# Optimization experiments

Hardware: AMD Instinct MI355X
Metric: run time of the kernel (lower is better)

The kernel has to match this reference:

```python
import jax, jax.numpy as jnp
import numpy as np

B, L, D, H, DK, DV, FF, V, N = 1, 1024, 1024, 16, 64, 64, 4096, 32000, 12


def _ln(x, s, b):
    mu = jnp.mean(x, axis=-1, keepdims=True)
    var = jnp.mean((x - mu) ** 2, axis=-1, keepdims=True)
    return (x - mu) / jnp.sqrt(var + 1e-5) * s + b


def _pe(length, d):
    # interleaved sin/cos positional encoding, matching stack([sin,cos],-1).view(L,D)
    i = 2.0 * jnp.arange(d // 2, dtype=jnp.float32)
    base = 10000.0 ** (-i / d)
    half = jnp.arange(length, dtype=jnp.float32)[:, None] * base[None, :]  # [L, D/2]
    return jnp.stack([jnp.sin(half), jnp.cos(half)], axis=-1).reshape(length, d)


def setup_inputs() -> dict:
    key = jax.random.key(0)
    ks = jax.random.split(key, 8)
    s = 0.02
    return {
        "tokens": jax.random.randint(ks[0], (B, L), 0, V),
        "emb": jax.random.normal(ks[1], (V, D), jnp.float32) * s,
        "final_b": jnp.zeros((V,), jnp.float32),
        "Wq": jax.random.normal(ks[2], (N, H, D, DK), jnp.float32) * s,
        "Wk": jax.random.normal(ks[3], (N, H, D, DK), jnp.float32) * s,
        "Wv": jax.random.normal(ks[4], (N, H, D, DV), jnp.float32) * s,
        "Wo": jax.random.normal(ks[5], (N, H * DV, D), jnp.float32) * s,
        "ln1_s": jnp.ones((N, D), jnp.float32),
        "ln1_b": jnp.zeros((N, D), jnp.float32),
        "W1": jax.random.normal(ks[6], (N, D, FF), jnp.float32) * s,
        "b1": jnp.zeros((N, FF), jnp.float32),
        "W2": jax.random.normal(ks[7], (N, FF, D), jnp.float32) * s,
        "b2": jnp.zeros((N, D), jnp.float32),
        "ln2_s": jnp.ones((N, D), jnp.float32),
        "ln2_b": jnp.zeros((N, D), jnp.float32),
    }


def _forward(tokens, emb, final_b, Wq, Wk, Wv, Wo, ln1_s, ln1_b, W1, b1, W2, b2, ln2_s, ln2_b):
    a = emb[tokens] * jnp.sqrt(jnp.float32(3.0 * D))  # tied-weight scaling
    a = a + (a + _pe(L, D))  # faithful to `a += pe(a)` where pe returns x + PE
    mask = jnp.tril(jnp.ones((L, L), dtype=bool))
    scale = 1.0 / jnp.sqrt(jnp.float32(D))  # original divides by sqrt(d_model), not d_k

    def layer(x, p):
        wq, wk, wv, wo, s1, sb1, w1, bb1, w2, bb2, s2, sb2 = p
        q = jnp.einsum('bld,hdk->bhlk', x, wq)
        k = jnp.einsum('bld,hdk->bhlk', x, wk)
        v = jnp.einsum('bld,hdv->bhlv', x, wv)
        scores = jnp.einsum('bhqk,bhmk->bhqm', q, k) * scale  # [B,H,L,L]
        scores = jnp.where(mask, scores, -jnp.inf)  # causal triu(-inf)
        attn = jax.nn.softmax(scores, axis=-1)
        o = jnp.einsum('bhqm,bhmv->bhqv', attn, v)
        o = o.transpose(0, 2, 1, 3).reshape(x.shape[0], L, H * DV)  # concat heads
        x = _ln(x + o @ wo, s1, sb1)  # post-LN residual
        f = jax.nn.relu(x @ w1 + bb1) @ w2 + bb2
        x = _ln(x + f, s2, sb2)
        return x, None

    x, _ = jax.lax.scan(layer, a, (Wq, Wk, Wv, Wo, ln1_s, ln1_b, W1, b1, W2, b2, ln2_s, ln2_b))
    return x @ emb.T + final_b  # tied output projection with bias


def reference(tokens, emb, final_b, Wq, Wk, Wv, Wo, ln1_s, ln1_b, W1, b1, W2, b2, ln2_s, ln2_b):
    return _forward(tokens, emb, final_b, Wq, Wk, Wv, Wo, ln1_s, ln1_b, W1, b1, W2, b2, ln2_s, ln2_b)
```

## Files before the change

kernel.cpp:

```cpp
#include <hip/hip_runtime.h>

typedef unsigned short u16;
typedef __attribute__((ext_vector_type(8))) short short8;
typedef __attribute__((ext_vector_type(4))) float f32x4;
typedef __attribute__((ext_vector_type(4))) u16 u16x4;

#define LSEQ   1024
#define DMODEL 1024
#define NHEAD  16
#define DHEAD  64
#define DFF    4096
#define NLAYER 12
#define NVOCAB 32000

__device__ __forceinline__ u16 f2b(float f) {
  union { float f; unsigned u; } x; x.f = f;
  unsigned r = x.u + 0x7fffu + ((x.u >> 16) & 1u);
  return (u16)(r >> 16);
}
__device__ __forceinline__ float b2f(u16 u) {
  union { unsigned u; float f; } x; x.u = ((unsigned)u) << 16; return x.f;
}

__device__ __forceinline__ f32x4 mfma16(short8 a, short8 b, f32x4 c) {
  return __builtin_amdgcn_mfma_f32_16x16x32_bf16(a, b, c, 0, 0, 0);
}

__device__ __forceinline__ void gload16(const u16* g, u16* l) {
  __builtin_amdgcn_global_load_lds(
      (const __attribute__((address_space(1))) void*)g,
      (__attribute__((address_space(3))) void*)l, 16, 0, 0);
}

template<int N> __device__ __forceinline__ void waitvm() {
  if constexpr (N <= 0)      asm volatile("s_waitcnt vmcnt(0)" ::: "memory");
  else if constexpr (N == 1) asm volatile("s_waitcnt vmcnt(1)" ::: "memory");
  else if constexpr (N == 2) asm volatile("s_waitcnt vmcnt(2)" ::: "memory");
  else if constexpr (N == 3) asm volatile("s_waitcnt vmcnt(3)" ::: "memory");
  else if constexpr (N == 4) asm volatile("s_waitcnt vmcnt(4)" ::: "memory");
  else if constexpr (N == 5) asm volatile("s_waitcnt vmcnt(5)" ::: "memory");
  else if constexpr (N == 6) asm volatile("s_waitcnt vmcnt(6)" ::: "memory");
  else                       asm volatile("s_waitcnt vmcnt(8)" ::: "memory");
}

__global__ __launch_bounds__(256) void embed_k(const int* __restrict__ tok,
    const float* __restrict__ emb, float* __restrict__ x, u16* __restrict__ xb)
{
  const int l = blockIdx.x;
  const int d0 = threadIdx.x * 4;
  const int t = tok[l];
  const float lf = (float)l;
  float o[4]; u16 obv[4];
#pragma unroll
  for (int j = 0; j < 4; ++j) {
    int d = d0 + j;
    int p = d >> 1;
    float ang = lf * powf(10000.0f, -(float)(2 * p) / 1024.0f);
    float pe = (d & 1) ? cosf(ang) : sinf(ang);
    float val = 2.0f * emb[(size_t)t * DMODEL + d] * 55.42562584220407f + pe;
    o[j] = val; obv[j] = f2b(val);
  }
  *reinterpret_cast<float4*>(x + (size_t)l * DMODEL + d0) = make_float4(o[0], o[1], o[2], o[3]);
  u16x4 vb = { obv[0], obv[1], obv[2], obv[3] };
  *reinterpret_cast<u16x4*>(xb + (size_t)l * DMODEL + d0) = vb;
}

__global__ __launch_bounds__(256) void ln_k(const float* __restrict__ xin,
    const float* __restrict__ ypart, int P, const float* __restrict__ ybias,
    const float* __restrict__ s, const float* __restrict__ b,
    float* __restrict__ xout, u16* __restrict__ xbout)
{
  const int row = blockIdx.x, tid = threadIdx.x;
  const int d0 = tid * 4;
  float4 xv = *reinterpret_cast<const float4*>(xin + (size_t)row * DMODEL + d0);
  float t0 = xv.x, t1 = xv.y, t2 = xv.z, t3 = xv.w;
#pragma unroll 2
  for (int p = 0; p < P; ++p) {
    float4 yv = *reinterpret_cast<const float4*>(ypart + (size_t)p * (LSEQ * DMODEL) + (size_t)row * DMODEL + d0);
    t0 += yv.x; t1 += yv.y; t2 += yv.z; t3 += yv.w;
  }
  if (ybias) {
    float4 bb = *reinterpret_cast<const float4*>(ybias + d0);
    t0 += bb.x; t1 += bb.y; t2 += bb.z; t3 += bb.w;
  }
  float sum = t0 + t1 + t2 + t3;
  float sq  = t0 * t0 + t1 * t1 + t2 * t2 + t3 * t3;
#pragma unroll
  for (int d = 1; d < 64; d <<= 1) { sum += __shfl_xor(sum, d); sq += __shfl_xor(sq, d); }
  __shared__ float ssum[4], ssq[4];
  const int wid = tid >> 6;
  if ((tid & 63) == 0) { ssum[wid] = sum; ssq[wid] = sq; }
  __syncthreads();
  sum = ssum[0] + ssum[1] + ssum[2] + ssum[3];
  sq  = ssq[0] + ssq[1] + ssq[2] + ssq[3];
  const float mu = sum * (1.0f / 1024.0f);
  const float var = sq * (1.0f / 1024.0f) - mu * mu;
  const float rstd = rsqrtf(var + 1e-5f);
  float4 sv = *reinterpret_cast<const float4*>(s + d0);
  float4 bv = *reinterpret_cast<const float4*>(b + d0);
  float o0 = (t0 - mu) * rstd * sv.x + bv.x;
  float o1 = (t1 - mu) * rstd * sv.y + bv.y;
  float o2 = (t2 - mu) * rstd * sv.z + bv.z;
  float o3 = (t3 - mu) * rstd * sv.w + bv.w;
  *reinterpret_cast<float4*>(xout + (size_t)row * DMODEL + d0) = make_float4(o0, o1, o2, o3);
  u16x4 vb = { f2b(o0), f2b(o1), f2b(o2), f2b(o3) };
  *reinterpret_cast<u16x4*>(xbout + (size_t)row * DMODEL + d0) = vb;
}

__global__ __launch_bounds__(256) void lnb_k(const float* __restrict__ xin,
    const u16* __restrict__ ypart, int P, const float* __restrict__ ybias,
    const float* __restrict__ s, const float* __restrict__ b,
    float* __restrict__ xout, u16* __restrict__ xbout)
{
  const int row = blockIdx.x, tid = threadIdx.x;
  const int d0 = tid * 4;
  float4 xv = *reinterpret_cast<const float4*>(xin + (size_t)row * DMODEL + d0);
  float t0 = xv.x, t1 = xv.y, t2 = xv.z, t3 = xv.w;
#pragma unroll 4
  for (int p = 0; p < P; ++p) {
    u16x4 yv = *reinterpret_cast<const u16x4*>(ypart + (size_t)p * (LSEQ * DMODEL) + (size_t)row * DMODEL + d0);
    t0 += b2f(yv[0]); t1 += b2f(yv[1]); t2 += b2f(yv[2]); t3 += b2f(yv[3]);
  }
  if (ybias) {
    float4 bb = *reinterpret_cast<const float4*>(ybias + d0);
    t0 += bb.x; t1 += bb.y; t2 += bb.z; t3 += bb.w;
  }
  float sum = t0 + t1 + t2 + t3;
  float sq  = t0 * t0 + t1 * t1 + t2 * t2 + t3 * t3;
#pragma unroll
  for (int d = 1; d < 64; d <<= 1) { sum += __shfl_xor(sum, d); sq += __shfl_xor(sq, d); }
  __shared__ float ssum[4], ssq[4];
  const int wid = tid >> 6;
  if ((tid & 63) == 0) { ssum[wid] = sum; ssq[wid] = sq; }
  __syncthreads();
  sum = ssum[0] + ssum[1] + ssum[2] + ssum[3];
  sq  = ssq[0] + ssq[1] + ssq[2] + ssq[3];
  const float mu = sum * (1.0f / 1024.0f);
  const float var = sq * (1.0f / 1024.0f) - mu * mu;
  const float rstd = rsqrtf(var + 1e-5f);
  float4 sv = *reinterpret_cast<const float4*>(s + d0);
  float4 bv = *reinterpret_cast<const float4*>(b + d0);
  float o0 = (t0 - mu) * rstd * sv.x + bv.x;
  float o1 = (t1 - mu) * rstd * sv.y + bv.y;
  float o2 = (t2 - mu) * rstd * sv.z + bv.z;
  float o3 = (t3 - mu) * rstd * sv.w + bv.w;
  *reinterpret_cast<float4*>(xout + (size_t)row * DMODEL + d0) = make_float4(o0, o1, o2, o3);
  u16x4 vb = { f2b(o0), f2b(o1), f2b(o2), f2b(o3) };
  *reinterpret_cast<u16x4*>(xbout + (size_t)row * DMODEL + d0) = vb;
}

__global__ __launch_bounds__(256) void ffred_k(const u16* __restrict__ sp,
    const float* __restrict__ bias, u16* __restrict__ out)
{
  const size_t idx = ((size_t)blockIdx.x * 256 + threadIdx.x) * 8;
  const int c0 = (int)(idx % DFF);
  short8 a = *reinterpret_cast<const short8*>(sp + idx);
  short8 b = *reinterpret_cast<const short8*>(sp + (size_t)LSEQ * DFF + idx);
  short8 o;
#pragma unroll
  for (int j = 0; j < 8; ++j) {
    float val = b2f((u16)a[j]) + b2f((u16)b[j]) + bias[c0 + j];
    o[j] = (short)f2b(fmaxf(val, 0.0f));
  }
  *reinterpret_cast<short8*>(out + idx) = o;
}

__global__ __launch_bounds__(256) void tconv_k(const float* __restrict__ in, u16* __restrict__ out,
                                               int R, int C, int zper, int lstride, int obase, int zstride)
{
  __shared__ float t[64][65];
  const int rt = blockIdx.y * 64, ct = blockIdx.x * 64;
  const int z = blockIdx.z;
  in += (size_t)z * zstride;
  const int tr = threadIdx.x >> 4, tc = threadIdx.x & 15;
#pragma unroll
  for (int i = 0; i < 4; ++i) {
    int r = i * 16 + tr;
    float4 v = *reinterpret_cast<const float4*>(in + (size_t)(rt + r) * C + ct + tc * 4);
    t[r][tc * 4 + 0] = v.x; t[r][tc * 4 + 1] = v.y;
    t[r][tc * 4 + 2] = v.z; t[r][tc * 4 + 3] = v.w;
  }
  __syncthreads();
  const size_t orow0 = (size_t)(z / zper) * lstride + (size_t)(z % zper) * C + obase + ct;
#pragma unroll
  for (int i = 0; i < 4; ++i) {
    int c = i * 16 + tr;
    u16x4 o;
    o[0] = f2b(t[tc * 4 + 0][c]); o[1] = f2b(t[tc * 4 + 1][c]);
    o[2] = f2b(t[tc * 4 + 2][c]); o[3] = f2b(t[tc * 4 + 3][c]);
    *reinterpret_cast<u16x4*>(out + (orow0 + c) * R + rt + tc * 4) = o;
  }
}

__global__ __launch_bounds__(256) void ec_k(const float* __restrict__ in, u16* __restrict__ out)
{
  const size_t i = ((size_t)blockIdx.x * 256 + threadIdx.x) * 8;
  float4 a = *reinterpret_cast<const float4*>(in + i);
  float4 b = *reinterpret_cast<const float4*>(in + i + 4);
  short8 o;
  o[0] = f2b(a.x); o[1] = f2b(a.y); o[2] = f2b(a.z); o[3] = f2b(a.w);
  o[4] = f2b(b.x); o[5] = f2b(b.y); o[6] = f2b(b.z); o[7] = f2b(b.w);
  *reinterpret_cast<short8*>(out + i) = o;
}

template<int BM, int BN, int BK, int BSRC, bool BIAS, bool RELU, int OUTMODE, int KSPLIT>
__global__ __launch_bounds__(256) void gemm_bt(
    const u16* __restrict__ A, int lda,
    const void* __restrict__ Bp, int ldb,
    const float* __restrict__ bias,
    void* __restrict__ Cv, int ldc, int Ktot)
{
  constexpr int CPR = BK / 8;
  constexpr int SWM = CPR - 1;
  constexpr int LA = (BM * CPR) / 256;
  constexpr int LB = (BN * CPR) / 256;
  constexpr int LT = LA + LB;
  __shared__ u16 As[3][BM * BK];
  __shared__ u16 Bs[3][BN * BK];
  const int tid = threadIdx.x, lane = tid & 63, wid = tid >> 6;
  const int nwg = gridDim.x * gridDim.y;
  const int flat = blockIdx.y * gridDim.x + blockIdx.x;
  const int qq = nwg >> 3;
  const int ni = (flat & 7) * qq + (flat >> 3);
  const int m0 = (ni % gridDim.x) * BM, n0 = (ni / gridDim.x) * BN;
  const int kbase = (KSPLIT > 1) ? blockIdx.z * (Ktot / KSPLIT) : 0;
  const int klen  = (KSPLIT > 1) ? (Ktot / KSPLIT) : Ktot;
  constexpr int FM = BM / 32, FN = BN / 32;
  constexpr int KS = BK / 32;
  const int wm = (wid >> 1) * (BM / 2), wn = (wid & 1) * (BN / 2);
  f32x4 acc[FM][FN] = {};

  if constexpr (BSRC == 0) {
    const u16* Bt = (const u16*)Bp;
    auto stage = [&](int slot, int k0) {
#pragma unroll
      for (int i = 0; i < LA; ++i) {
        int c = i * 256 + tid;
        int row = c / CPR, p0 = c % CPR;
        int part = p0 ^ (((row * CPR) >> 3) & SWM);
        gload16(A + (size_t)(m0 + row) * lda + k0 + part * 8,
                &As[slot][(i * 256 + wid * 64) * 8]);
      }
#pragma unroll
      for (int i = 0; i < LB; ++i) {
        int c = i * 256 + tid;
        int row = c / CPR, p0 = c % CPR;
        int part = p0 ^ (((row * CPR) >> 3) & SWM);
        gload16(Bt + (size_t)(n0 + row) * ldb + k0 + part * 8,
                &Bs[slot][(i * 256 + wid * 64) * 8]);
      }
    };

    const int NT = klen / BK;
    stage(0, kbase);
    stage(1, kbase + BK);
    waitvm<LT>();
    __builtin_amdgcn_s_barrier();
    asm volatile("" ::: "memory");

    int cur = 0, stg = 2;
    for (int t = 0; t < NT; ++t) {
      const bool more = (t + 2 < NT);
      if (more) stage(stg, kbase + (t + 2) * BK);
      asm volatile("" ::: "memory");
      short8 a[KS][FM], b[KS][FN];
#pragma unroll
      for (int ks = 0; ks < KS; ++ks) {
#pragma unroll
        for (int fm = 0; fm < FM; ++fm) {
          int row = wm + fm * 16 + (lane & 15);
          int pidx = (ks * 4 + (lane >> 4)) ^ (((row * CPR) >> 3) & SWM);
          a[ks][fm] = *reinterpret_cast<const short8*>(&As[cur][row * BK + pidx * 8]);
        }
#pragma unroll
        for (int fn = 0; fn < FN; ++fn) {
          int row = wn + fn * 16 + (lane & 15);
          int pidx = (ks * 4 + (lane >> 4)) ^ (((row * CPR) >> 3) & SWM);
          b[ks][fn] = *reinterpret_cast<const short8*>(&Bs[cur][row * BK + pidx * 8]);
        }
      }
#pragma unroll
      for (int ks = 0; ks < KS; ++ks)
#pragma unroll
        for (int fm = 0; fm < FM; ++fm)
#pragma unroll
          for (int fn = 0; fn < FN; ++fn)
            acc[fm][fn] = mfma16(a[ks][fm], b[ks][fn], acc[fm][fn]);
      if (more) waitvm<LT>(); else waitvm<0>();
      __builtin_amdgcn_s_barrier();
      asm volatile("" ::: "memory");
      cur = (cur == 2) ? 0 : cur + 1;
      stg = (stg == 2) ? 0 : stg + 1;
    }
  } else {
    const float* Bf = (const float*)Bp;
    for (int k0 = 0; k0 < Ktot; k0 += BK) {
#pragma unroll
      for (int i = 0; i < LA; ++i) {
        int c = i * 256 + tid;
        int row = c / CPR, part = c % CPR;
        gload16(A + (size_t)(m0 + row) * lda + k0 + part * 8,
                &As[0][(i * 256 + wid * 64) * 8]);
      }
      {
        int row = tid >> 1, kh = (tid & 1) * 16;
        const float* src = Bf + (size_t)(n0 + row) * ldb + k0 + kh;
        float4 v0 = *reinterpret_cast<const float4*>(src);
        float4 v1 = *reinterpret_cast<const float4*>(src + 4);
        float4 v2 = *reinterpret_cast<const float4*>(src + 8);
        float4 v3 = *reinterpret_cast<const float4*>(src + 12);
        short8 p0, p1;
        p0[0] = f2b(v0.x); p0[1] = f2b(v0.y); p0[2] = f2b(v0.z); p0[3] = f2b(v0.w);
        p0[4] = f2b(v1.x); p0[5] = f2b(v1.y); p0[6] = f2b(v1.z); p0[7] = f2b(v1.w);
        p1[0] = f2b(v2.x); p1[1] = f2b(v2.y); p1[2] = f2b(v2.z); p1[3] = f2b(v2.w);
        p1[4] = f2b(v3.x); p1[5] = f2b(v3.y); p1[6] = f2b(v3.z); p1[7] = f2b(v3.w);
        *reinterpret_cast<short8*>(&Bs[0][row * BK + kh])     = p0;
        *reinterpret_cast<short8*>(&Bs[0][row * BK + kh + 8]) = p1;
      }
      __syncthreads();
      short8 a[KS][FM], b[KS][FN];
#pragma unroll
      for (int ks = 0; ks < KS; ++ks) {
#pragma unroll
        for (int fm = 0; fm < FM; ++fm) {
          int row = wm + fm * 16 + (lane & 15);
          a[ks][fm] = *reinterpret_cast<const short8*>(&As[0][row * BK + (ks * 4 + (lane >> 4)) * 8]);
        }
#pragma unroll
        for (int fn = 0; fn < FN; ++fn) {
          int row = wn + fn * 16 + (lane & 15);
          b[ks][fn] = *reinterpret_cast<const short8*>(&Bs[0][row * BK + (ks * 4 + (lane >> 4)) * 8]);
        }
      }
#pragma unroll
      for (int ks = 0; ks < KS; ++ks)
#pragma unroll
        for (int fm = 0; fm < FM; ++fm)
#pragma unroll
          for (int fn = 0; fn < FN; ++fn)
            acc[fm][fn] = mfma16(a[ks][fm], b[ks][fn], acc[fm][fn]);
      __syncthreads();
    }
  }

  const size_t pbase = (KSPLIT > 1) ? (size_t)blockIdx.z * gridDim.x * BM * ldc : 0;
#pragma unroll
  for (int fm = 0; fm < FM; ++fm) {
#pragma unroll
    for (int fn = 0; fn < FN; ++fn) {
#pragma unroll
      for (int r = 0; r < 4; ++r) {
        int row = m0 + wm + fm * 16 + (lane >> 4) * 4 + r;
        int col = n0 + wn + fn * 16 + (lane & 15);
        float val = acc[fm][fn][r];
        if (BIAS) val += bias[col];
        if (RELU) val = fmaxf(val, 0.0f);
        if (OUTMODE == 0) {
          ((float*)Cv)[pbase + (size_t)row * ldc + col] = val;
        } else if (OUTMODE == 1) {
          ((u16*)Cv)[(size_t)row * ldc + col] = f2b(val);
        } else if (OUTMODE == 3) {
          ((u16*)Cv)[pbase + (size_t)row * ldc + col] = f2b(val);
        } else {
          int sel = col >> 10, cc = col & 1023;
          if (sel == 0) val *= 0.03125f;
          ((u16*)Cv)[(size_t)sel * (LSEQ * DMODEL) + (size_t)row * DMODEL + cc] = f2b(val);
        }
      }
    }
  }
}

template<int FUSE>
__global__ __launch_bounds__(256) void attn_k(const u16* __restrict__ q,
    const u16* __restrict__ kmat, const u16* __restrict__ v, u16* __restrict__ o)
{
  __shared__ u16 Ks[64][72];
  __shared__ u16 Vt[64][72];
  __shared__ u16 Pl[4][16][72];
  const int tid = threadIdx.x, lane = tid & 63, wid = tid >> 6;
  const int h = blockIdx.y, qt = blockIdx.x;
  const int qw0 = qt * 64 + wid * 16;
  const int qrow = qw0 + (lane & 15);
  const size_t PLQ = (size_t)LSEQ * 3072;
  short8 aq0, aq1;
  if constexpr (FUSE) {
    const u16* qp = q + (size_t)qrow * 3072 + h * DHEAD + (lane >> 4) * 8;
    short8 a0 = *reinterpret_cast<const short8*>(qp);
    short8 b0 = *reinterpret_cast<const short8*>(qp + PLQ);
    short8 a1 = *reinterpret_cast<const short8*>(qp + 32);
    short8 b1 = *reinterpret_cast<const short8*>(qp + 32 + PLQ);
#pragma unroll
    for (int j = 0; j < 8; ++j) {
      aq0[j] = (short)f2b((b2f((u16)a0[j]) + b2f((u16)b0[j])) * 0.03125f);
      aq1[j] = (short)f2b((b2f((u16)a1[j]) + b2f((u16)b1[j])) * 0.03125f);
    }
  } else {
    aq0 = *reinterpret_cast<const short8*>(q + (size_t)qrow * DMODEL + h * DHEAD + (lane >> 4) * 8);
    aq1 = *reinterpret_cast<const short8*>(q + (size_t)qrow * DMODEL + h * DHEAD + 32 + (lane >> 4) * 8);
  }
  float m_run[4], l_run[4];
  f32x4 oacc[4] = {};
#pragma unroll
  for (int r = 0; r < 4; ++r) { m_run[r] = -1e30f; l_run[r] = 0.0f; }
  const int kvend = qt * 64 + 64;

  const int kvi = tid >> 2, c16 = (tid & 3) * 16;
  short8 kr0, kr1, vr0, vr1;
  short8 kr0b, kr1b, vr0b, vr1b;
  auto loadregs = [&](int kv0) {
    if constexpr (FUSE) {
      const u16* kp = q + (size_t)(kv0 + kvi) * 3072 + 1024 + h * DHEAD + c16;
      kr0  = *reinterpret_cast<const short8*>(kp);
      kr1  = *reinterpret_cast<const short8*>(kp + 8);
      kr0b = *reinterpret_cast<const short8*>(kp + PLQ);
      kr1b = *reinterpret_cast<const short8*>(kp + 8 + PLQ);
      const u16* vp = q + (size_t)(kv0 + kvi) * 3072 + 2048 + h * DHEAD + c16;
      vr0  = *reinterpret_cast<const short8*>(vp);
      vr1  = *reinterpret_cast<const short8*>(vp + 8);
      vr0b = *reinterpret_cast<const short8*>(vp + PLQ);
      vr1b = *reinterpret_cast<const short8*>(vp + 8 + PLQ);
    } else {
      const u16* kp = kmat + (size_t)(kv0 + kvi) * DMODEL + h * DHEAD + c16;
      kr0 = *reinterpret_cast<const short8*>(kp);
      kr1 = *reinterpret_cast<const short8*>(kp + 8);
      const u16* vp = v + (size_t)(kv0 + kvi) * DMODEL + h * DHEAD + c16;
      vr0 = *reinterpret_cast<const short8*>(vp);
      vr1 = *reinterpret_cast<const short8*>(vp + 8);
    }
  };
  loadregs(0);

  for (int kv0 = 0; kv0 < kvend; kv0 += 64) {
    __syncthreads();
    if constexpr (FUSE) {
      short8 ko0, ko1;
#pragma unroll
      for (int j = 0; j < 8; ++j) {
        ko0[j] = (short)f2b(b2f((u16)kr0[j]) + b2f((u16)kr0b[j]));
        ko1[j] = (short)f2b(b2f((u16)kr1[j]) + b2f((u16)kr1b[j]));
      }
      *reinterpret_cast<short8*>(&Ks[kvi][c16])     = ko0;
      *reinterpret_cast<short8*>(&Ks[kvi][c16 + 8]) = ko1;
#pragma unroll
      for (int j = 0; j < 8; ++j) {
        Vt[c16 + j][kvi]     = f2b(b2f((u16)vr0[j]) + b2f((u16)vr0b[j]));
        Vt[c16 + 8 + j][kvi] = f2b(b2f((u16)vr1[j]) + b2f((u16)vr1b[j]));
      }
    } else {
      *reinterpret_cast<short8*>(&Ks[kvi][c16])     = kr0;
      *reinterpret_cast<short8*>(&Ks[kvi][c16 + 8]) = kr1;
#pragma unroll
      for (int j = 0; j < 8; ++j) { Vt[c16 + j][kvi] = (u16)vr0[j]; Vt[c16 + 8 + j][kvi] = (u16)vr1[j]; }
    }
    __syncthreads();
    if (kv0 + 64 < kvend) loadregs(kv0 + 64);

    float sm[4][4];
#pragma unroll
    for (int t2 = 0; t2 < 4; ++t2) {
      short8 bk0 = *reinterpret_cast<const short8*>(&Ks[t2 * 16 + (lane & 15)][(lane >> 4) * 8]);
      short8 bk1 = *reinterpret_cast<const short8*>(&Ks[t2 * 16 + (lane & 15)][32 + (lane >> 4) * 8]);
      f32x4 s4 = {};
      s4 = mfma16(aq0, bk0, s4);
      s4 = mfma16(aq1, bk1, s4);
#pragma unroll
      for (int r = 0; r < 4; ++r) {
        int rowg = qw0 + (lane >> 4) * 4 + r;
        int colg = kv0 + t2 * 16 + (lane & 15);
        sm[t2][r] = (colg <= rowg) ? s4[r] : -1e30f;
      }
    }
    float alpha[4], p[4][4];
#pragma unroll
    for (int r = 0; r < 4; ++r) {
      float mx = fmaxf(fmaxf(sm[0][r], sm[1][r]), fmaxf(sm[2][r], sm[3][r]));
#pragma unroll
      for (int d = 1; d < 16; d <<= 1) mx = fmaxf(mx, __shfl_xor(mx, d));
      float mn = fmaxf(m_run[r], mx);
      alpha[r] = __expf(m_run[r] - mn);
      float ps = 0.0f;
#pragma unroll
      for (int t2 = 0; t2 < 4; ++t2) { p[t2][r] = __expf(sm[t2][r] - mn); ps += p[t2][r]; }
#pragma unroll
      for (int d = 1; d < 16; d <<= 1) ps += __shfl_xor(ps, d);
      l_run[r] = l_run[r] * alpha[r] + ps;
      m_run[r] = mn;
    }
#pragma unroll
    for (int fn = 0; fn < 4; ++fn) {
      f32x4 t = oacc[fn];
      t[0] *= alpha[0]; t[1] *= alpha[1]; t[2] *= alpha[2]; t[3] *= alpha[3];
      oacc[fn] = t;
    }
#pragma unroll
    for (int r = 0; r < 4; ++r) {
      int rit = (lane >> 4) * 4 + r;
#pragma unroll
      for (int t2 = 0; t2 < 4; ++t2)
        Pl[wid][rit][t2 * 16 + (lane & 15)] = f2b(p[t2][r]);
    }
    short8 pa0 = *reinterpret_cast<const short8*>(&Pl[wid][lane & 15][(lane >> 4) * 8]);
    short8 pa1 = *reinterpret_cast<const short8*>(&Pl[wid][lane & 15][32 + (lane >> 4) * 8]);
#pragma unroll
    for (int fn = 0; fn < 4; ++fn) {
      short8 bv0 = *reinterpret_cast<const short8*>(&Vt[fn * 16 + (lane & 15)][(lane >> 4) * 8]);
      short8 bv1 = *reinterpret_cast<const short8*>(&Vt[fn * 16 + (lane & 15)][32 + (lane >> 4) * 8]);
      oacc[fn] = mfma16(pa0, bv0, oacc[fn]);
      oacc[fn] = mfma16(pa1, bv1, oacc[fn]);
    }
  }
#pragma unroll
  for (int fn = 0; fn < 4; ++fn) {
#pragma unroll
    for (int r = 0; r < 4; ++r) {
      int row = qw0 + (lane >> 4) * 4 + r;
      float val = oacc[fn][r] / l_run[r];
      o[(size_t)row * DMODEL + h * DHEAD + fn * 16 + (lane & 15)] = f2b(val);
    }
  }
}

extern "C" void kernel_launch(void* const* d_in, const int* in_sizes, int n_in,
                              void* d_out, int out_size, void* d_ws, size_t ws_size,
                              hipStream_t stream) {
  (void)in_sizes; (void)n_in; (void)out_size;
  const int*   tok    = (const int*)d_in[0];
  const float* emb    = (const float*)d_in[1];
  const float* finalb = (const float*)d_in[2];
  const float* Wq     = (const float*)d_in[3];
  const float* Wk     = (const float*)d_in[4];
  const float* Wv     = (const float*)d_in[5];
  const float* Wo     = (const float*)d_in[6];
  const float* ln1s   = (const float*)d_in[7];
  const float* ln1b   = (const float*)d_in[8];
  const float* W1     = (const float*)d_in[9];
  const float* b1     = (const float*)d_in[10];
  const float* W2     = (const float*)d_in[11];
  const float* b2     = (const float*)d_in[12];
  const float* ln2s   = (const float*)d_in[13];
  const float* ln2b   = (const float*)d_in[14];
  float* out = (float*)d_out;

  float* x   = (float*)d_ws;
  float* y   = x + LSEQ * DMODEL;
  u16* xb    = (u16*)(y + LSEQ * DMODEL);
  u16* qb    = xb + LSEQ * DMODEL;
  u16* kb    = qb + LSEQ * DMODEL;
  u16* vb    = kb + LSEQ * DMODEL;
  u16* ob    = vb + LSEQ * DMODEL;
  u16* h1    = ob + LSEQ * DMODEL;
  u16* wbase = h1 + LSEQ * DFF;
  float* woPart = (float*)h1;

  const size_t eQKV = (size_t)3 * DMODEL * DMODEL;
  const size_t eWO  = (size_t)DMODEL * DMODEL;
  const size_t eW1  = (size_t)DFF * DMODEL;
  const size_t eW2  = (size_t)DMODEL * DFF;
  const size_t perL = eQKV + eWO + eW1 + eW2;
  const size_t eEMB = (size_t)NVOCAB * DMODEL;
  const size_t eSP  = (size_t)2 * LSEQ * DFF;
  const size_t actE = (size_t)(wbase - (u16*)d_ws);
  const size_t bigNeed = (actE + NLAYER * perL + eEMB + eSP) * 2;
  const size_t midNeed = (actE + perL + eEMB) * 2;
  const int mode = ws_size >= bigNeed ? 2 : (ws_size >= midNeed ? 1 : 0);
  const int WL = (mode == 2) ? NLAYER : 1;

  u16* qkvT = wbase;
  u16* woT  = qkvT + WL * eQKV;
  u16* w1T  = woT  + WL * eWO;
  u16* w2T  = w1T  + WL * eW1;
  u16* embT = w2T  + WL * eW2;
  u16* sp   = embT + eEMB;

  if (mode == 2) {
    tconv_k<<<dim3(1, 16, 192), 256, 0, stream>>>(Wq, qkvT, DMODEL, DHEAD, 16, 3 * DMODEL, 0,    DMODEL * DHEAD);
    tconv_k<<<dim3(1, 16, 192), 256, 0, stream>>>(Wk, qkvT, DMODEL, DHEAD, 16, 3 * DMODEL, 1024, DMODEL * DHEAD);
    tconv_k<<<dim3(1, 16, 192), 256, 0, stream>>>(Wv, qkvT, DMODEL, DHEAD, 16, 3 * DMODEL, 2048, DMODEL * DHEAD);
    tconv_k<<<dim3(16, 16, 12), 256, 0, stream>>>(Wo, woT, DMODEL, DMODEL, 1, DMODEL, 0, DMODEL * DMODEL);
    tconv_k<<<dim3(64, 16, 12), 256, 0, stream>>>(W1, w1T, DMODEL, DFF, 1, DFF, 0, DMODEL * DFF);
    tconv_k<<<dim3(16, 64, 12), 256, 0, stream>>>(W2, w2T, DFF, DMODEL, 1, DMODEL, 0, DFF * DMODEL);
    ec_k<<<(NVOCAB * DMODEL) / 2048, 256, 0, stream>>>(emb, embT);
  } else if (mode == 1) {
    ec_k<<<(NVOCAB * DMODEL) / 2048, 256, 0, stream>>>(emb, embT);
  }

  embed_k<<<LSEQ, 256, 0, stream>>>(tok, emb, x, xb);

  for (int l = 0; l < NLAYER; ++l) {
    const float* wq  = Wq + (size_t)l * NHEAD * DMODEL * DHEAD;
    const float* wk  = Wk + (size_t)l * NHEAD * DMODEL * DHEAD;
    const float* wv  = Wv + (size_t)l * NHEAD * DMODEL * DHEAD;
    const float* wo  = Wo + (size_t)l * DMODEL * DMODEL;
    const float* w1  = W1 + (size_t)l * DMODEL * DFF;
    const float* b1l = b1 + (size_t)l * DFF;
    const float* w2  = W2 + (size_t)l * DFF * DMODEL;
    const float* b2l = b2 + (size_t)l * DMODEL;
    u16* qkvTl = qkvT + (mode == 2 ? (size_t)l * eQKV : 0);
    u16* woTl  = woT  + (mode == 2 ? (size_t)l * eWO  : 0);
    u16* w1Tl  = w1T  + (mode == 2 ? (size_t)l * eW1  : 0);
    u16* w2Tl  = w2T  + (mode == 2 ? (size_t)l * eW2  : 0);

    if (mode < 2) {
      tconv_k<<<dim3(1, 16, 16), 256, 0, stream>>>(wq, qkvTl, DMODEL, DHEAD, 16, 0, 0,    DMODEL * DHEAD);
      tconv_k<<<dim3(1, 16, 16), 256, 0, stream>>>(wk, qkvTl, DMODEL, DHEAD, 16, 0, 1024, DMODEL * DHEAD);
      tconv_k<<<dim3(1, 16, 16), 256, 0, stream>>>(wv, qkvTl, DMODEL, DHEAD, 16, 0, 2048, DMODEL * DHEAD);
      tconv_k<<<dim3(16, 16, 1), 256, 0, stream>>>(wo, woTl, DMODEL, DMODEL, 1, 0, 0, 0);
      tconv_k<<<dim3(64, 16, 1), 256, 0, stream>>>(w1, w1Tl, DMODEL, DFF, 1, 0, 0, 0);
      tconv_k<<<dim3(16, 64, 1), 256, 0, stream>>>(w2, w2Tl, DFF, DMODEL, 1, 0, 0, 0);
    }

    if (mode == 2) {
      gemm_bt<128, 128, 32, 0, false, false, 3, 2><<<dim3(8, 24, 2), 256, 0, stream>>>(
          xb, DMODEL, qkvTl, DMODEL, nullptr, sp, 3 * DMODEL, DMODEL);
      attn_k<1><<<dim3(16, 16), 256, 0, stream>>>(sp, nullptr, nullptr, ob);
    } else {
      gemm_bt<64, 64, 64, 0, false, false, 2, 1><<<dim3(16, 48), 256, 0, stream>>>(
          xb, DMODEL, qkvTl, DMODEL, nullptr, qb, DMODEL, DMODEL);
      attn_k<0><<<dim3(16, 16), 256, 0, stream>>>(qb, kb, vb, ob);
    }
    gemm_bt<64, 64, 64, 0, false, false, 0, 2><<<dim3(16, 16, 2), 256, 0, stream>>>(
        ob, DMODEL, woTl, DMODEL, nullptr, woPart, DMODEL, DMODEL);
    ln_k<<<LSEQ, 256, 0, stream>>>(x, woPart, 2, nullptr,
        ln1s + (size_t)l * DMODEL, ln1b + (size_t)l * DMODEL, x, xb);
    if (mode == 2) {
      gemm_bt<128, 128, 32, 0, false, false, 3, 2><<<dim3(8, 32, 2), 256, 0, stream>>>(
          xb, DMODEL, w1Tl, DMODEL, nullptr, sp, DFF, DMODEL);
      ffred_k<<<(LSEQ * DFF) / 2048, 256, 0, stream>>>(sp, b1l, h1);
      gemm_bt<128, 128, 32, 0, false, false, 3, 8><<<dim3(8, 8, 8), 256, 0, stream>>>(
          h1, DFF, w2Tl, DFF, nullptr, sp, DMODEL, DFF);
      lnb_k<<<LSEQ, 256, 0, stream>>>(x, sp, 8, b2l,
          ln2s + (size_t)l * DMODEL, ln2b + (size_t)l * DMODEL, x, xb);
    } else {
      gemm_bt<64, 64, 64, 0, true, true, 1, 1><<<dim3(16, 64), 256, 0, stream>>>(
          xb, DMODEL, w1Tl, DMODEL, b1l, h1, DFF, DMODEL);
      gemm_bt<64, 64, 64, 0, false, false, 0, 2><<<dim3(16, 16, 2), 256, 0, stream>>>(
          h1, DFF, w2Tl, DFF, nullptr, (float*)qb, DMODEL, DFF);
      ln_k<<<LSEQ, 256, 0, stream>>>(x, (float*)qb, 2, b2l,
          ln2s + (size_t)l * DMODEL, ln2b + (size_t)l * DMODEL, x, xb);
    }
  }

  if (mode >= 1) {
    gemm_bt<128, 128, 32, 0, true, false, 0, 1><<<dim3(8, 250), 256, 0, stream>>>(
        xb, DMODEL, embT, DMODEL, finalb, out, NVOCAB, DMODEL);
  } else {
    gemm_bt<128, 128, 32, 1, true, false, 0, 1><<<dim3(8, 250), 256, 0, stream>>>(
        xb, DMODEL, emb, DMODEL, finalb, out, NVOCAB, DMODEL);
  }
}
```

Baseline: 1.790 ms.

## Fuse FFN split-K reduction, bias and ReLU into W2 GEMM A-operand load

Removes the separate ffred kernel by adding a GEMM variant that loads both split-K partials of the W1 output from global memory and adds bias and ReLU in registers. It then writes the result into shared memory as the A operand of the W2 GEMM, alongside async B staging. The Wo projection also moves to the 128x128 split-K-8 bf16 path with lnb_k, replacing the 64x64 fp32 two-way split. This saves one kernel launch and an h1 round trip, but the W2 GEMM redoes the A-side reduction for every N tile (8x) and uses synchronous register loads for A.

After: 1.915 ms. 1.07x slower.

```diff
diff --git a/kernel.cpp b/kernel.cpp
--- a/kernel.cpp
+++ b/kernel.cpp
@@ -33,14 +33,16 @@
 }
 
 template<int N> __device__ __forceinline__ void waitvm() {
-  if constexpr (N <= 0)      asm volatile("s_waitcnt vmcnt(0)" ::: "memory");
-  else if constexpr (N == 1) asm volatile("s_waitcnt vmcnt(1)" ::: "memory");
-  else if constexpr (N == 2) asm volatile("s_waitcnt vmcnt(2)" ::: "memory");
-  else if constexpr (N == 3) asm volatile("s_waitcnt vmcnt(3)" ::: "memory");
-  else if constexpr (N == 4) asm volatile("s_waitcnt vmcnt(4)" ::: "memory");
-  else if constexpr (N == 5) asm volatile("s_waitcnt vmcnt(5)" ::: "memory");
-  else if constexpr (N == 6) asm volatile("s_waitcnt vmcnt(6)" ::: "memory");
-  else                       asm volatile("s_waitcnt vmcnt(8)" ::: "memory");
+  if constexpr (N <= 0)       asm volatile("s_waitcnt vmcnt(0)" ::: "memory");
+  else if constexpr (N == 1)  asm volatile("s_waitcnt vmcnt(1)" ::: "memory");
+  else if constexpr (N == 2)  asm volatile("s_waitcnt vmcnt(2)" ::: "memory");
+  else if constexpr (N == 3)  asm volatile("s_waitcnt vmcnt(3)" ::: "memory");
+  else if constexpr (N == 4)  asm volatile("s_waitcnt vmcnt(4)" ::: "memory");
+  else if constexpr (N == 5)  asm volatile("s_waitcnt vmcnt(5)" ::: "memory");
+  else if constexpr (N == 6)  asm volatile("s_waitcnt vmcnt(6)" ::: "memory");
+  else if constexpr (N == 8)  asm volatile("s_waitcnt vmcnt(8)" ::: "memory");
+  else if constexpr (N == 10) asm volatile("s_waitcnt vmcnt(10)" ::: "memory");
+  else                        asm volatile("s_waitcnt vmcnt(12)" ::: "memory");
 }
 
 __global__ __launch_bounds__(256) void embed_k(const int* __restrict__ tok,
@@ -147,22 +149,6 @@
   *reinterpret_cast<float4*>(xout + (size_t)row * DMODEL + d0) = make_float4(o0, o1, o2, o3);
   u16x4 vb = { f2b(o0), f2b(o1), f2b(o2), f2b(o3) };
   *reinterpret_cast<u16x4*>(xbout + (size_t)row * DMODEL + d0) = vb;
-}
-
-__global__ __launch_bounds__(256) void ffred_k(const u16* __restrict__ sp,
-    const float* __restrict__ bias, u16* __restrict__ out)
-{
-  const size_t idx = ((size_t)blockIdx.x * 256 + threadIdx.x) * 8;
-  const int c0 = (int)(idx % DFF);
-  short8 a = *reinterpret_cast<const short8*>(sp + idx);
-  short8 b = *reinterpret_cast<const short8*>(sp + (size_t)LSEQ * DFF + idx);
-  short8 o;
-#pragma unroll
-  for (int j = 0; j < 8; ++j) {
-    float val = b2f((u16)a[j]) + b2f((u16)b[j]) + bias[c0 + j];
-    o[j] = (short)f2b(fmaxf(val, 0.0f));
-  }
-  *reinterpret_cast<short8*>(out + idx) = o;
 }
 
 __global__ __launch_bounds__(256) void tconv_k(const float* __restrict__ in, u16* __restrict__ out,
@@ -292,6 +278,99 @@
       cur = (cur == 2) ? 0 : cur + 1;
       stg = (stg == 2) ? 0 : stg + 1;
     }
+  } else if constexpr (BSRC == 2) {
+    const u16* Bt = (const u16*)Bp;
+    const u16* P0 = A;
+    const u16* P1 = A + (size_t)LSEQ * lda;
+    short8 rA[LA];
+    auto loadA = [&](int k0) {
+#pragma unroll
+      for (int i = 0; i < LA; ++i) {
+        int c = i * 256 + tid;
+        int row = c / CPR, p0c = c % CPR;
+        int part = p0c ^ (((row * CPR) >> 3) & SWM);
+        size_t off = (size_t)(m0 + row) * lda + k0 + part * 8;
+        short8 a0 = *reinterpret_cast<const short8*>(&P0[off]);
+        short8 a1 = *reinterpret_cast<const short8*>(&P1[off]);
+        float4 bb0 = *reinterpret_cast<const float4*>(&bias[k0 + part * 8]);
+        float4 bb1 = *reinterpret_cast<const float4*>(&bias[k0 + part * 8 + 4]);
+        short8 o;
+        o[0] = (short)f2b(fmaxf(b2f((u16)a0[0]) + b2f((u16)a1[0]) + bb0.x, 0.0f));
+        o[1] = (short)f2b(fmaxf(b2f((u16)a0[1]) + b2f((u16)a1[1]) + bb0.y, 0.0f));
+        o[2] = (short)f2b(fmaxf(b2f((u16)a0[2]) + b2f((u16)a1[2]) + bb0.z, 0.0f));
+        o[3] = (short)f2b(fmaxf(b2f((u16)a0[3]) + b2f((u16)a1[3]) + bb0.w, 0.0f));
+        o[4] = (short)f2b(fmaxf(b2f((u16)a0[4]) + b2f((u16)a1[4]) + bb1.x, 0.0f));
+        o[5] = (short)f2b(fmaxf(b2f((u16)a0[5]) + b2f((u16)a1[5]) + bb1.y, 0.0f));
+        o[6] = (short)f2b(fmaxf(b2f((u16)a0[6]) + b2f((u16)a1[6]) + bb1.z, 0.0f));
+        o[7] = (short)f2b(fmaxf(b2f((u16)a0[7]) + b2f((u16)a1[7]) + bb1.w, 0.0f));
+        rA[i] = o;
+      }
+    };
+    auto writeA = [&](int slot) {
+#pragma unroll
+      for (int i = 0; i < LA; ++i) {
+        int c = i * 256 + tid;
+        *reinterpret_cast<short8*>(&As[slot][c * 8]) = rA[i];
+      }
+    };
+    auto stageB = [&](int slot, int k0) {
+#pragma unroll
+      for (int i = 0; i < LB; ++i) {
+        int c = i * 256 + tid;
+        int row = c / CPR, p0c = c % CPR;
+        int part = p0c ^ (((row * CPR) >> 3) & SWM);
+        gload16(Bt + (size_t)(n0 + row) * ldb + k0 + part * 8,
+                &Bs[slot][(i * 256 + wid * 64) * 8]);
+      }
+    };
+    const int NT = klen / BK;
+    loadA(kbase);          writeA(0);
+    loadA(kbase + BK);     writeA(1);
+    stageB(0, kbase);
+    stageB(1, kbase + BK);
+    loadA(kbase + 2 * BK);
+    waitvm<8>();
+    asm volatile("s_waitcnt lgkmcnt(0)" ::: "memory");
+    __builtin_amdgcn_s_barrier();
+    asm volatile("" ::: "memory");
+
+    int cur = 0, stg = 2;
+    for (int t = 0; t < NT; ++t) {
+      const bool more = (t + 2 < NT);
+      if (more) writeA(stg);
+      if (t + 3 < NT) loadA(kbase + (t + 3) * BK);
+      if (more) stageB(stg, kbase + (t + 2) * BK);
+      asm volatile("" ::: "memory");
+      short8 a[KS][FM], b[KS][FN];
+#pragma unroll
+      for (int ks = 0; ks < KS; ++ks) {
+#pragma unroll
+        for (int fm = 0; fm < FM; ++fm) {
+          int row = wm + fm * 16 + (lane & 15);
+          int pidx = (ks * 4 + (lane >> 4)) ^ (((row * CPR) >> 3) & SWM);
+          a[ks][fm] = *reinterpret_cast<const short8*>(&As[cur][row * BK + pidx * 8]);
+        }
+#pragma unroll
+        for (int fn = 0; fn < FN; ++fn) {
+          int row = wn + fn * 16 + (lane & 15);
+          int pidx = (ks * 4 + (lane >> 4)) ^ (((row * CPR) >> 3) & SWM);
+          b[ks][fn] = *reinterpret_cast<const short8*>(&Bs[cur][row * BK + pidx * 8]);
+        }
+      }
+#pragma unroll
+      for (int ks = 0; ks < KS; ++ks)
+#pragma unroll
+        for (int fm = 0; fm < FM; ++fm)
+#pragma unroll
+          for (int fn = 0; fn < FN; ++fn)
+            acc[fm][fn] = mfma16(a[ks][fm], b[ks][fn], acc[fm][fn]);
+      if (more) waitvm<10>(); else waitvm<0>();
+      asm volatile("s_waitcnt lgkmcnt(0)" ::: "memory");
+      __builtin_amdgcn_s_barrier();
+      asm volatile("" ::: "memory");
+      cur = (cur == 2) ? 0 : cur + 1;
+      stg = (stg == 2) ? 0 : stg + 1;
+    }
   } else {
     const float* Bf = (const float*)Bp;
     for (int k0 = 0; k0 < Ktot; k0 += BK) {
@@ -551,7 +630,7 @@
   u16* ob    = vb + LSEQ * DMODEL;
   u16* h1    = ob + LSEQ * DMODEL;
   u16* wbase = h1 + LSEQ * DFF;
-  float* woPart = (float*)h1;
+  u16* ff2p  = qb;
 
   const size_t eQKV = (size_t)3 * DMODEL * DMODEL;
   const size_t eWO  = (size_t)DMODEL * DMODEL;
@@ -614,24 +693,24 @@
       gemm_bt<128, 128, 32, 0, false, false, 3, 2><<<dim3(8, 24, 2), 256, 0, stream>>>(
           xb, DMODEL, qkvTl, DMODEL, nullptr, sp, 3 * DMODEL, DMODEL);
       attn_k<1><<<dim3(16, 16), 256, 0, stream>>>(sp, nullptr, nullptr, ob);
+      gemm_bt<128, 128, 32, 0, false, false, 3, 8><<<dim3(8, 8, 8), 256, 0, stream>>>(
+          ob, DMODEL, woTl, DMODEL, nullptr, sp, DMODEL, DMODEL);
+      lnb_k<<<LSEQ, 256, 0, stream>>>(x, sp, 8, nullptr,
+          ln1s + (size_t)l * DMODEL, ln1b + (size_t)l * DMODEL, x, xb);
+      gemm_bt<128, 128, 32, 0, false, false, 3, 2><<<dim3(8, 32, 2), 256, 0, stream>>>(
+          xb, DMODEL, w1Tl, DMODEL, nullptr, sp, DFF, DMODEL);
+      gemm_bt<128, 128, 32, 2, false, false, 3, 8><<<dim3(8, 8, 8), 256, 0, stream>>>(
+          sp, DFF, w2Tl, DFF, b1l, ff2p, DMODEL, DFF);
+      lnb_k<<<LSEQ, 256, 0, stream>>>(x, ff2p, 8, b2l,
+          ln2s + (size_t)l * DMODEL, ln2b + (size_t)l * DMODEL, x, xb);
     } else {
       gemm_bt<64, 64, 64, 0, false, false, 2, 1><<<dim3(16, 48), 256, 0, stream>>>(
           xb, DMODEL, qkvTl, DMODEL, nullptr, qb, DMODEL, DMODEL);
       attn_k<0><<<dim3(16, 16), 256, 0, stream>>>(qb, kb, vb, ob);
-    }
-    gemm_bt<64, 64, 64, 0, false, false, 0, 2><<<dim3(16, 16, 2), 256, 0, stream>>>(
-        ob, DMODEL, woTl, DMODEL, nullptr, woPart, DMODEL, DMODEL);
-    ln_k<<<LSEQ, 256, 0, stream>>>(x, woPart, 2, nullptr,
-        ln1s + (size_t)l * DMODEL, ln1b + (size_t)l * DMODEL, x, xb);
-    if (mode == 2) {
-      gemm_bt<128, 128, 32, 0, false, false, 3, 2><<<dim3(8, 32, 2), 256, 0, stream>>>(
-          xb, DMODEL, w1Tl, DMODEL, nullptr, sp, DFF, DMODEL);
-      ffred_k<<<(LSEQ * DFF) / 2048, 256, 0, stream>>>(sp, b1l, h1);
-      gemm_bt<128, 128, 32, 0, false, false, 3, 8><<<dim3(8, 8, 8), 256, 0, stream>>>(
-          h1, DFF, w2Tl, DFF, nullptr, sp, DMODEL, DFF);
-      lnb_k<<<LSEQ, 256, 0, stream>>>(x, sp, 8, b2l,
-          ln2s + (size_t)l * DMODEL, ln2b + (size_t)l * DMODEL, x, xb);
-    } else {
+      gemm_bt<64, 64, 64, 0, false, false, 0, 2><<<dim3(16, 16, 2), 256, 0, stream>>>(
+          ob, DMODEL, woTl, DMODEL, nullptr, (float*)h1, DMODEL, DMODEL);
+      ln_k<<<LSEQ, 256, 0, stream>>>(x, (float*)h1, 2, nullptr,
+          ln1s + (size_t)l * DMODEL, ln1b + (size_t)l * DMODEL, x, xb);
       gemm_bt<64, 64, 64, 0, true, true, 1, 1><<<dim3(16, 64), 256, 0, stream>>>(
           xb, DMODEL, w1Tl, DMODEL, b1l, h1, DFF, DMODEL);
       gemm_bt<64, 64, 64, 0, false, false, 0, 2><<<dim3(16, 16, 2), 256, 0, stream>>>(
```
